# Performance work log

Hardware: AMD Instinct MI355X
Metric: run time of the kernel (lower is better)

Reference implementation:

```python
import jax, jax.numpy as jnp
import numpy as np

NUM_CLASSES = 20
NUM_ANCHORS = 5
INPUT_SIZE = 320.0
CONF_THR = 0.5
IOU_THR = 0.5
EPS = 1e-6
H = W = 40


def setup_inputs() -> dict:
    key = jax.random.key(0)
    x = jax.random.normal(key, (1, NUM_ANCHORS * (5 + NUM_CLASSES), H, W), dtype=jnp.float32)
    scaled_anchors = jnp.array(
        [[1.3221, 1.73145], [3.19275, 4.00944], [5.05587, 8.09892],
         [9.47112, 4.84053], [11.2364, 10.0071]], dtype=jnp.float32)
    return {"x": x, "scaled_anchors": scaled_anchors}


def decode(x, anchors):
    # x: (B, A*(5+C), H, W) -> boxes (B, A*H*W, 6) = [cx, cy, w, h, conf, cls]
    B, _, h, w = x.shape
    A = anchors.shape[0]
    stride_h = INPUT_SIZE / h
    stride_w = INPUT_SIZE / w
    pred = x.reshape(B, A, 5 + NUM_CLASSES, h, w).transpose(0, 1, 3, 4, 2)  # (B,A,H,W,5+C)
    tx = jax.nn.sigmoid(pred[..., 0])
    ty = jax.nn.sigmoid(pred[..., 1])
    tw = pred[..., 2]
    th = pred[..., 3]
    conf = jax.nn.sigmoid(pred[..., 4])
    cls_idx = jnp.argmax(jax.nn.sigmoid(pred[..., 5:]), axis=-1)  # (B,A,H,W)
    grid_x = jnp.arange(w, dtype=x.dtype)            # broadcasts along last axis
    grid_y = jnp.arange(h, dtype=x.dtype)[:, None]   # broadcasts along row axis
    aw = anchors[:, 0][None, :, None, None]
    ah = anchors[:, 1][None, :, None, None]
    bx = (tx + grid_x) * stride_w
    by = (ty + grid_y) * stride_h
    bw = jnp.exp(tw) * aw * stride_w
    bh = jnp.exp(th) * ah * stride_h
    boxes = jnp.stack([bx, by, bw, bh, conf], axis=-1).reshape(B, -1, 5)
    cls_f = cls_idx.reshape(B, -1, 1).astype(x.dtype)
    return jnp.concatenate([boxes, cls_f], axis=-1)


def nms(boxes6):
    # boxes6: (N, 6) [cx, cy, w, h, conf, cls]. Fixed-shape NMS: boxes are
    # sorted by conf desc; suppressed / low-conf boxes are zeroed out.
    order = jnp.argsort(-boxes6[:, 4])
    b = boxes6[order]
    valid = b[:, 4] > CONF_THR
    cx, cy, w, h, cls = b[:, 0], b[:, 1], b[:, 2], b[:, 3], b[:, 5]
    x1, y1 = cx - w / 2.0, cy - h / 2.0
    x2, y2 = cx + w / 2.0, cy + h / 2.0
    inter_w = jnp.clip(jnp.minimum(x2[:, None], x2[None, :]) - jnp.maximum(x1[:, None], x1[None, :]), 0)
    inter_h = jnp.clip(jnp.minimum(y2[:, None], y2[None, :]) - jnp.maximum(y1[:, None], y1[None, :]), 0)
    inter = inter_w * inter_h                       # (N, N)
    area = jnp.abs((x2 - x1) * (y2 - y1))
    iou = inter / (area[:, None] + area[None, :] - inter + EPS)
    N = b.shape[0]
    idx = jnp.arange(N)

    def body(i, keep):
        # kept box i suppresses later boxes of the same class with IoU >= thr
        sup = keep[i] & keep & (cls == cls[i]) & (iou[i] >= IOU_THR) & (idx > i)
        return keep & ~sup

    keep = jax.lax.fori_loop(0, N, body, valid)
    return b * keep[:, None].astype(b.dtype)


def reference(x, scaled_anchors):
    dec = decode(x, scaled_anchors)   # (1, N, 6)
    return nms(dec[0])                # (N, 6)
```

## Files before the change

kernel.cpp:

```cpp
#include <hip/hip_runtime.h>
#include <stdint.h>

#define NBOX 8000
#define NPAD 8192

#define ECNT_OFF 0
#define SB(i)    (0x10000 + (size_t)(i) * 0x8000)
#define EDGE_OFF (size_t)0x200000

__device__ __forceinline__ float sigmoidf_(float x) {
    return 1.0f / (1.0f + expf(-x));
}

__global__ __launch_bounds__(512) void sort_decode_kernel(const float* __restrict__ x,
                                                          const float* __restrict__ anchors,
                                                          unsigned char* __restrict__ ws) {
    __shared__ unsigned long long keys[NPAD];
    __shared__ int partial[512];
    int tid  = threadIdx.x;
    int lane = tid & 63;
    int wv   = tid >> 6;
    int b    = blockIdx.x;

    if (b == 0 && tid == 0) *(unsigned int*)(ws + ECNT_OFF) = 0u;

    for (int t = tid; t < NPAD; t += 512) {
        unsigned long long k;
        if (t < NBOX) {
            int a = t / 1600, pos = t - a * 1600;
            float c = sigmoidf_(x[a * 40000 + 4 * 1600 + pos]);
            k = ((unsigned long long)__float_as_uint(c) << 32) | (unsigned long long)(8191 - t);
        } else {
            k = (unsigned long long)(8191 - t);
        }
        keys[t] = k;
    }
    __syncthreads();

    int i = (b << 6) + lane;
    unsigned long long ki = keys[i];
    const unsigned long long* ks = &keys[wv << 10];
    int cnt = 0;
    #pragma unroll 8
    for (int jj = 0; jj < 1024; ++jj) cnt += (ks[jj] > ki) ? 1 : 0;
    partial[(wv << 6) + lane] = cnt;
    __syncthreads();

    if (wv == 0) {
        int r = 0;
        #pragma unroll
        for (int s = 0; s < 8; ++s) r += partial[(s << 6) + lane];

        float bx = 0.f, by = 0.f, bw = 0.f, bh = 0.f, conf = 0.f, cls = -1.0f;
        if (i < NBOX) {
            int a = i / 1600, pos = i - a * 1600;
            int gy = pos / 40, gx = pos - gy * 40;
            const float* p = x + (size_t)a * 40000 + pos;
            float tx = sigmoidf_(p[0]);
            float ty = sigmoidf_(p[1600]);
            float tw = p[2 * 1600];
            float th = p[3 * 1600];
            conf = sigmoidf_(p[4 * 1600]);
            float best = -1.0f; int bi = 0;
            #pragma unroll
            for (int c = 0; c < 20; ++c) {
                float v = sigmoidf_(p[(5 + c) * 1600]);
                if (v > best) { best = v; bi = c; }
            }
            float aw = anchors[a * 2 + 0];
            float ah = anchors[a * 2 + 1];
            bx = (tx + (float)gx) * 8.0f;
            by = (ty + (float)gy) * 8.0f;
            bw = expf(tw) * aw * 8.0f;
            bh = expf(th) * ah * 8.0f;
            cls = (float)bi;
        }
        {
        #pragma clang fp contract(off)
            float x1 = bx - bw / 2.0f, y1 = by - bh / 2.0f;
            float x2 = bx + bw / 2.0f, y2 = by + bh / 2.0f;
            float ar = fabsf((x2 - x1) * (y2 - y1));
            ((float*)(ws + SB(0)))[r]  = bx;  ((float*)(ws + SB(1)))[r]  = by;
            ((float*)(ws + SB(2)))[r]  = bw;  ((float*)(ws + SB(3)))[r]  = bh;
            ((float*)(ws + SB(4)))[r]  = conf; ((float*)(ws + SB(5)))[r] = cls;
            ((float*)(ws + SB(6)))[r]  = x1;  ((float*)(ws + SB(7)))[r]  = y1;
            ((float*)(ws + SB(8)))[r]  = x2;  ((float*)(ws + SB(9)))[r]  = y2;
            ((float*)(ws + SB(10)))[r] = ar;
        }
    }
}

__global__ __launch_bounds__(256) void mask_kernel(unsigned char* __restrict__ ws) {
#pragma clang fp contract(off)
    const float* sconf = (const float*)(ws + SB(4));
    int i0 = blockIdx.y * 256;
    int w  = blockIdx.x;
    int j0 = w * 64;
    if (sconf[i0] <= 0.5f) return;
    if (sconf[j0] <= 0.5f) return;
    if (j0 + 64 <= i0) return;
    int tid  = threadIdx.x;
    int lane = tid & 63;
    int i    = i0 + tid;

    const float* sx1 = (const float*)(ws + SB(6));
    const float* sy1 = (const float*)(ws + SB(7));
    const float* sx2 = (const float*)(ws + SB(8));
    const float* sy2 = (const float*)(ws + SB(9));
    const float* sar = (const float*)(ws + SB(10));
    const float* scl = (const float*)(ws + SB(5));

    __shared__ float cx1[64], cy1[64], cx2[64], cy2[64], car[64], ccl[64], ccf[64];
    if (tid < 64) {
        int j = j0 + tid;
        cx1[tid] = sx1[j]; cy1[tid] = sy1[j];
        cx2[tid] = sx2[j]; cy2[tid] = sy2[j];
        car[tid] = sar[j]; ccl[tid] = scl[j]; ccf[tid] = sconf[j];
    }
    __syncthreads();

    unsigned long long word = 0;
    if (sconf[i] > 0.5f && j0 + 64 > i + 1) {
        float x1i = sx1[i], y1i = sy1[i], x2i = sx2[i], y2i = sy2[i];
        float ai = sar[i], ci = scl[i];
        for (int jj = 0; jj < 64; ++jj) {
            int j = j0 + jj;
            if (j <= i) continue;
            if (ccf[jj] <= 0.5f) continue;
            if (ccl[jj] != ci) continue;
            float iw = fminf(x2i, cx2[jj]) - fmaxf(x1i, cx1[jj]);
            iw = fmaxf(iw, 0.0f);
            float ih = fminf(y2i, cy2[jj]) - fmaxf(y1i, cy1[jj]);
            ih = fmaxf(ih, 0.0f);
            float inter = iw * ih;
            float denom = ai + car[jj] - inter + 1e-6f;
            if (inter / denom >= 0.5f) word |= (1ull << jj);
        }
    }

    int pc = __popcll(word);
    int scan = pc;
    #pragma unroll
    for (int d = 1; d < 64; d <<= 1) {
        int t = __shfl_up(scan, d, 64);
        if (lane >= d) scan += t;
    }
    int total = __shfl(scan, 63, 64);
    if (total > 0) {
        unsigned int base = 0;
        if (lane == 63)
            base = atomicAdd((unsigned int*)(ws + ECNT_OFF), (unsigned int)total);
        base = (unsigned int)__shfl((int)base, 63, 64);
        unsigned int off = base + (unsigned int)(scan - pc);
        unsigned int* edges = (unsigned int*)(ws + EDGE_OFF);
        unsigned long long t = word;
        while (t) {
            int bit = __builtin_ctzll(t);
            t &= t - 1ull;
            edges[off++] = ((unsigned int)i << 13) | (unsigned int)(j0 + bit);
        }
    }
}

__global__ __launch_bounds__(1024, 1) void nms_out_kernel(unsigned char* __restrict__ ws,
                                                          float* __restrict__ out) {
    int tid  = threadIdx.x;
    int lane = tid & 63;
    unsigned int E = *(const unsigned int*)(ws + ECNT_OFF);
    const unsigned int* edges = (const unsigned int*)(ws + EDGE_OFF);
    const float* sconf = (const float*)(ws + SB(4));

    __shared__ unsigned long long valid[128], alive[128], supp[128];
    __shared__ int flag;

    for (int c = tid >> 6; c < 128; c += 16) {
        unsigned long long m = __ballot(sconf[(c << 6) + lane] > 0.5f);
        if (lane == 0) valid[c] = m;
    }
    __syncthreads();
    if (tid < 128) alive[tid] = valid[tid];
    __syncthreads();

    for (;;) {
        if (tid < 128) supp[tid] = 0ull;
        __syncthreads();
        for (unsigned int e = tid; e < E; e += 1024) {
            unsigned int u = edges[e];
            unsigned int i = u >> 13, j = u & 8191u;
            if ((alive[i >> 6] >> (i & 63)) & 1ull)
                atomicOr(&supp[j >> 6], 1ull << (j & 63));
        }
        if (tid == 0) flag = 0;
        __syncthreads();
        if (tid < 128) {
            unsigned long long na = valid[tid] & ~supp[tid];
            if (na != alive[tid]) { alive[tid] = na; flag = 1; }
        }
        __syncthreads();
        if (!flag) break;
    }

    for (int r = tid; r < NBOX; r += 1024) {
        bool keep = (alive[r >> 6] >> (r & 63)) & 1ull;
        float o0 = 0.f, o1 = 0.f, o2 = 0.f, o3 = 0.f, o4 = 0.f, o5 = 0.f;
        if (keep) {
            o0 = ((const float*)(ws + SB(0)))[r];
            o1 = ((const float*)(ws + SB(1)))[r];
            o2 = ((const float*)(ws + SB(2)))[r];
            o3 = ((const float*)(ws + SB(3)))[r];
            o4 = ((const float*)(ws + SB(4)))[r];
            o5 = ((const float*)(ws + SB(5)))[r];
        }
        out[r * 6 + 0] = o0;
        out[r * 6 + 1] = o1;
        out[r * 6 + 2] = o2;
        out[r * 6 + 3] = o3;
        out[r * 6 + 4] = o4;
        out[r * 6 + 5] = o5;
    }
}

extern "C" void kernel_launch(void* const* d_in, const int* in_sizes, int n_in,
                              void* d_out, int out_size, void* d_ws, size_t ws_size,
                              hipStream_t stream) {
    const float* x       = (const float*)d_in[0];
    const float* anchors = (const float*)d_in[1];
    float* out           = (float*)d_out;
    unsigned char* ws    = (unsigned char*)d_ws;

    sort_decode_kernel<<<NPAD / 64, 512, 0, stream>>>(x, anchors, ws);
    dim3 mgrid(128, NPAD / 256);
    mask_kernel<<<mgrid, 256, 0, stream>>>(ws);
    nms_out_kernel<<<1, 1024, 0, stream>>>(ws, out);
}
```

Measured before the change: 119.1 us.

## Ballot-based rank counting, LDS-cached edge list, and parallel output kernel

The rank-counting sort now holds 16 key chunks in registers and counts larger keys with wave ballots and popcounts over 32 broadcast keys per block, doubling the grid to 256 blocks. The single-block NMS fixpoint loop caches the edge list in LDS when it fits, so repeated passes stop re-reading global memory. The output scatter moves out of the single-block kernel into a separate 32-block kernel that stages rows in shared memory for coalesced stores. This adds a fourth launch and a 128 KB LDS buffer in the NMS kernel.

```diff
diff --git a/kernel.cpp b/kernel.cpp
--- a/kernel.cpp
+++ b/kernel.cpp
@@ -5,6 +5,7 @@
 #define NPAD 8192
 
 #define ECNT_OFF 0
+#define ALIVE_OFF 0x1000
 #define SB(i)    (0x10000 + (size_t)(i) * 0x8000)
 #define EDGE_OFF (size_t)0x200000
 
@@ -16,7 +17,7 @@
                                                           const float* __restrict__ anchors,
                                                           unsigned char* __restrict__ ws) {
     __shared__ unsigned long long keys[NPAD];
-    __shared__ int partial[512];
+    __shared__ int partial[256];
     int tid  = threadIdx.x;
     int lane = tid & 63;
     int wv   = tid >> 6;
@@ -37,20 +38,31 @@
     }
     __syncthreads();
 
-    int i = (b << 6) + lane;
-    unsigned long long ki = keys[i];
-    const unsigned long long* ks = &keys[wv << 10];
-    int cnt = 0;
-    #pragma unroll 8
-    for (int jj = 0; jj < 1024; ++jj) cnt += (ks[jj] > ki) ? 1 : 0;
-    partial[(wv << 6) + lane] = cnt;
-    __syncthreads();
-
-    if (wv == 0) {
+    unsigned long long kj[16];
+    #pragma unroll
+    for (int c = 0; c < 16; ++c) kj[c] = keys[(wv << 10) + (c << 6) + lane];
+    unsigned long long ki = keys[(b << 5) + lane];
+
+    int vout = 0;
+    for (int ii = 0; ii < 32; ++ii) {
+        unsigned int klo = (unsigned int)__builtin_amdgcn_readlane((int)(unsigned int)ki, ii);
+        unsigned int khi = (unsigned int)__builtin_amdgcn_readlane((int)(unsigned int)(ki >> 32), ii);
+        unsigned long long kib = ((unsigned long long)khi << 32) | (unsigned long long)klo;
+        int c = 0;
+        #pragma unroll
+        for (int ch = 0; ch < 16; ++ch)
+            c += __popcll(__ballot(kj[ch] > kib));
+        vout = (lane == ii) ? c : vout;
+    }
+    if (lane < 32) partial[(wv << 5) + lane] = vout;
+    __syncthreads();
+
+    if (wv == 0 && lane < 32) {
         int r = 0;
         #pragma unroll
-        for (int s = 0; s < 8; ++s) r += partial[(s << 6) + lane];
-
+        for (int s = 0; s < 8; ++s) r += partial[(s << 5) + lane];
+
+        int i = (b << 5) + lane;
         float bx = 0.f, by = 0.f, bw = 0.f, bh = 0.f, conf = 0.f, cls = -1.0f;
         if (i < NBOX) {
             int a = i / 1600, pos = i - a * 1600;
@@ -162,8 +174,8 @@
     }
 }
 
-__global__ __launch_bounds__(1024, 1) void nms_out_kernel(unsigned char* __restrict__ ws,
-                                                          float* __restrict__ out) {
+#define ELDS 32768
+__global__ __launch_bounds__(1024, 1) void nms_kernel(unsigned char* __restrict__ ws) {
     int tid  = threadIdx.x;
     int lane = tid & 63;
     unsigned int E = *(const unsigned int*)(ws + ECNT_OFF);
@@ -172,11 +184,15 @@
 
     __shared__ unsigned long long valid[128], alive[128], supp[128];
     __shared__ int flag;
+    __shared__ unsigned int eld[ELDS];
 
     for (int c = tid >> 6; c < 128; c += 16) {
         unsigned long long m = __ballot(sconf[(c << 6) + lane] > 0.5f);
         if (lane == 0) valid[c] = m;
     }
+    bool uselds = (E <= (unsigned int)ELDS);
+    if (uselds)
+        for (unsigned int e = tid; e < E; e += 1024) eld[e] = edges[e];
     __syncthreads();
     if (tid < 128) alive[tid] = valid[tid];
     __syncthreads();
@@ -184,11 +200,20 @@
     for (;;) {
         if (tid < 128) supp[tid] = 0ull;
         __syncthreads();
-        for (unsigned int e = tid; e < E; e += 1024) {
-            unsigned int u = edges[e];
-            unsigned int i = u >> 13, j = u & 8191u;
-            if ((alive[i >> 6] >> (i & 63)) & 1ull)
-                atomicOr(&supp[j >> 6], 1ull << (j & 63));
+        if (uselds) {
+            for (unsigned int e = tid; e < E; e += 1024) {
+                unsigned int u = eld[e];
+                unsigned int i = u >> 13, j = u & 8191u;
+                if ((alive[i >> 6] >> (i & 63)) & 1ull)
+                    atomicOr(&supp[j >> 6], 1ull << (j & 63));
+            }
+        } else {
+            for (unsigned int e = tid; e < E; e += 1024) {
+                unsigned int u = edges[e];
+                unsigned int i = u >> 13, j = u & 8191u;
+                if ((alive[i >> 6] >> (i & 63)) & 1ull)
+                    atomicOr(&supp[j >> 6], 1ull << (j & 63));
+            }
         }
         if (tid == 0) flag = 0;
         __syncthreads();
@@ -200,23 +225,34 @@
         if (!flag) break;
     }
 
-    for (int r = tid; r < NBOX; r += 1024) {
-        bool keep = (alive[r >> 6] >> (r & 63)) & 1ull;
-        float o0 = 0.f, o1 = 0.f, o2 = 0.f, o3 = 0.f, o4 = 0.f, o5 = 0.f;
-        if (keep) {
-            o0 = ((const float*)(ws + SB(0)))[r];
-            o1 = ((const float*)(ws + SB(1)))[r];
-            o2 = ((const float*)(ws + SB(2)))[r];
-            o3 = ((const float*)(ws + SB(3)))[r];
-            o4 = ((const float*)(ws + SB(4)))[r];
-            o5 = ((const float*)(ws + SB(5)))[r];
-        }
-        out[r * 6 + 0] = o0;
-        out[r * 6 + 1] = o1;
-        out[r * 6 + 2] = o2;
-        out[r * 6 + 3] = o3;
-        out[r * 6 + 4] = o4;
-        out[r * 6 + 5] = o5;
+    if (tid < 128) ((unsigned long long*)(ws + ALIVE_OFF))[tid] = alive[tid];
+}
+
+__global__ __launch_bounds__(256) void out_kernel(const unsigned char* __restrict__ ws,
+                                                  float* __restrict__ out) {
+    __shared__ float o[256 * 6];
+    int tid = threadIdx.x;
+    int r0  = blockIdx.x << 8;
+    int r   = r0 + tid;
+    const unsigned long long* alive = (const unsigned long long*)(ws + ALIVE_OFF);
+
+    float v0 = 0.f, v1 = 0.f, v2 = 0.f, v3 = 0.f, v4 = 0.f, v5 = 0.f;
+    if (r < NBOX && ((alive[r >> 6] >> (r & 63)) & 1ull)) {
+        v0 = ((const float*)(ws + SB(0)))[r];
+        v1 = ((const float*)(ws + SB(1)))[r];
+        v2 = ((const float*)(ws + SB(2)))[r];
+        v3 = ((const float*)(ws + SB(3)))[r];
+        v4 = ((const float*)(ws + SB(4)))[r];
+        v5 = ((const float*)(ws + SB(5)))[r];
+    }
+    o[tid * 6 + 0] = v0; o[tid * 6 + 1] = v1; o[tid * 6 + 2] = v2;
+    o[tid * 6 + 3] = v3; o[tid * 6 + 4] = v4; o[tid * 6 + 5] = v5;
+    __syncthreads();
+
+    int base = r0 * 6;
+    for (int t = tid; t < 256 * 6; t += 256) {
+        int idx = base + t;
+        if (idx < NBOX * 6) out[idx] = o[t];
     }
 }
 
@@ -228,8 +264,9 @@
     float* out           = (float*)d_out;
     unsigned char* ws    = (unsigned char*)d_ws;
 
-    sort_decode_kernel<<<NPAD / 64, 512, 0, stream>>>(x, anchors, ws);
+    sort_decode_kernel<<<NPAD / 32, 512, 0, stream>>>(x, anchors, ws);
     dim3 mgrid(128, NPAD / 256);
     mask_kernel<<<mgrid, 256, 0, stream>>>(ws);
-    nms_out_kernel<<<1, 1024, 0, stream>>>(ws, out);
-}
+    nms_kernel<<<1, 1024, 0, stream>>>(ws);
+    out_kernel<<<32, 256, 0, stream>>>(ws, out);
+}
```

Result: faster. 111.0 us (-6.8%).
